# Optimization experiments

Hardware: AMD Instinct MI355X
Metric: run time of the kernel (lower is better)

The kernel has to match this reference:

```python
import jax, jax.numpy as jnp
import numpy as np

B, T, F = 256, 512, 8
H = 512
OUT = 96


def setup_inputs() -> dict:
    key = jax.random.key(0)
    ks = jax.random.split(key, 7)
    stdv = 1.0 / np.sqrt(H)
    u = lambda k, shape, s: jax.random.uniform(k, shape, jnp.float32, -s, s)
    return {
        "x": jax.random.normal(ks[0], (B, T, F), jnp.float32),
        "weight_ih": u(ks[1], (3 * H, F), stdv),
        "weight_hh": u(ks[2], (3 * H, H), stdv),
        "bias_ih": u(ks[3], (3 * H,), stdv),
        "bias_hh": u(ks[4], (3 * H,), stdv),
        "fc_w": u(ks[5], (OUT, H), 1.0 / np.sqrt(H)),
        "fc_b": u(ks[6], (OUT,), 1.0 / np.sqrt(H)),
    }


def _gru_last_hidden(x, weight_ih, weight_hh, bias_ih, bias_hh):
    # x: [B, T, F] (batch_first). Precompute input projections for all steps.
    xt = jnp.swapaxes(x, 0, 1)                      # [T, B, F]
    x_res = jnp.einsum('tbf,gf->tbg', xt, weight_ih) + bias_ih  # [T, B, 3H]
    h0 = jnp.zeros((x.shape[0], weight_hh.shape[1]), x.dtype)   # [B, H]

    def step(h, xr):
        h_res = h @ weight_hh.T + bias_hh           # [B, 3H]
        i_r, i_z, i_n = jnp.split(xr, 3, axis=1)
        h_r, h_z, h_n = jnp.split(h_res, 3, axis=1)
        r = jax.nn.sigmoid(i_r + h_r)
        z = jax.nn.sigmoid(i_z + h_z)
        n = jnp.tanh(i_n + r * h_n)
        h_new = n - n * z + z * h                   # = (1-z)*n + z*h
        return h_new, None

    h_last, _ = jax.lax.scan(step, h0, x_res)
    return h_last                                    # [B, H]


def reference(x, weight_ih, weight_hh, bias_ih, bias_hh, fc_w, fc_b):
    h_last = _gru_last_hidden(x, weight_ih, weight_hh, bias_ih, bias_hh)
    return h_last @ fc_w.T + fc_b                    # [B, OUT]
```

## Files before the change

kernel.cpp:

```cpp
#include <hip/hip_runtime.h>
#include <hip/hip_bf16.h>

#define B_ 256
#define T_ 512
#define F_ 8
#define H_ 512
#define OUT_ 96

#define NCL 16
#define BT 16
#define NWG 8

typedef __attribute__((ext_vector_type(8))) short short8;
typedef __attribute__((ext_vector_type(4))) float f32x4;

__device__ unsigned long long g_hbuf[2ull * 64 * 256 * 2];
__device__ __align__(64) unsigned g_flag[NCL * 16];

__device__ __forceinline__ short f2bf(float v) {
  __hip_bfloat16 b = __float2bfloat16(v);
  unsigned short u;
  __builtin_memcpy(&u, &b, 2);
  return (short)u;
}

__device__ __forceinline__ size_t hidx(int buf, int chunk, int row) {
  return ((size_t)((buf * 64 + chunk) * 256 + row)) * 2;
}

__global__ void init_flags() {
  int i = blockIdx.x * 256 + (int)threadIdx.x;
  if (i < NCL * 16) g_flag[i] = 0;
}

__global__ __launch_bounds__(256, 1) void gru_persistent(
    const float* x, const float* w_ih, const float* w_hh,
    const float* bias_ih, const float* bias_hh,
    const float* fc_w, const float* fc_b, float* out) {
  const int tid = (int)threadIdx.x;
  const int w = tid >> 6;
  const int lane = tid & 63;
  const int l15 = lane & 15;
  const int lg = lane >> 4;
  const int bid = (int)blockIdx.x;
  const int cl = bid & 15;
  const int wgj = bid >> 4;
  const int rb0 = cl * BT;
  const int c0 = wgj * 64 + w * 16;

  __shared__ short8 h_lds[1024];
  __shared__ short t_h[16][68];

  short8 wfrag[3][17];
#pragma unroll
  for (int g = 0; g < 3; ++g) {
    const float* wr = w_hh + (size_t)(g * H_ + c0 + l15) * H_ + lg * 8;
#pragma unroll
    for (int kk = 0; kk < 16; ++kk) {
      f32x4 a = ((const f32x4*)(wr + kk * 32))[0];
      f32x4 b2 = ((const f32x4*)(wr + kk * 32))[1];
      short8 o;
#pragma unroll
      for (int j = 0; j < 4; ++j) { o[j] = f2bf(a[j]); o[4 + j] = f2bf(b2[j]); }
      wfrag[g][kk] = o;
    }
    short8 o = {0, 0, 0, 0, 0, 0, 0, 0};
    if (lg == 0) {
      const f32x4* wi = (const f32x4*)(w_ih + (size_t)(g * H_ + c0 + l15) * F_);
      f32x4 a = wi[0], b2 = wi[1];
#pragma unroll
      for (int j = 0; j < 4; ++j) { o[j] = f2bf(a[j]); o[4 + j] = f2bf(b2[j]); }
    }
    wfrag[g][16] = o;
  }

  const int colh = c0 + l15;
  const float b_r = bias_ih[colh] + bias_hh[colh];
  const float b_z = bias_ih[H_ + colh] + bias_hh[H_ + colh];
  const float bin_ = bias_ih[2 * H_ + colh];
  const float bhn_ = bias_hh[2 * H_ + colh];

  float hown[4] = {0.f, 0.f, 0.f, 0.f};
  bool gaveup = false;

  const int hrow = rb0 + l15;
  const float* xrow = x + (size_t)hrow * T_ * F_;

  f32x4 xa = ((const f32x4*)xrow)[0];
  f32x4 xb2 = ((const f32x4*)xrow)[1];

  for (int t = 0; t < T_; ++t) {
    if (t > 0) {
      if (!gaveup) {
        unsigned spins = 0;
        for (;;) {
          unsigned f = __hip_atomic_load(&g_flag[cl * 16 + (lane & 7)],
                                         __ATOMIC_RELAXED, __HIP_MEMORY_SCOPE_AGENT);
          if (__all((int)(f >= (unsigned)t))) break;
          __builtin_amdgcn_s_sleep(2);
          if (++spins > (1u << 20)) { gaveup = true; break; }
        }
        __builtin_amdgcn_sched_barrier(0);
      }
      const int buf = t & 1;
#pragma unroll
      for (int r4 = 0; r4 < 4; ++r4) {
        const int idx = r4 * 256 + tid;
        const int chunk = idx >> 4;
        const int lr = idx & 15;
        size_t i0 = hidx(buf, chunk, rb0 + lr);
        unsigned long long q0 = __hip_atomic_load(&g_hbuf[i0], __ATOMIC_RELAXED,
                                                  __HIP_MEMORY_SCOPE_AGENT);
        unsigned long long q1 = __hip_atomic_load(&g_hbuf[i0 + 1], __ATOMIC_RELAXED,
                                                  __HIP_MEMORY_SCOPE_AGENT);
        union { unsigned long long q[2]; short8 s; } u;
        u.q[0] = q0; u.q[1] = q1;
        h_lds[idx] = u.s;
      }
    }

    short8 xf;
#pragma unroll
    for (int j = 0; j < 4; ++j) { xf[j] = f2bf(xa[j]); xf[4 + j] = f2bf(xb2[j]); }

    __syncthreads();

    {
      const int tn = (t + 1 < T_) ? t + 1 : T_ - 1;
      xa = ((const f32x4*)(xrow + (size_t)tn * F_))[0];
      xb2 = ((const f32x4*)(xrow + (size_t)tn * F_))[1];
    }

    f32x4 acc_r = {0.f, 0.f, 0.f, 0.f}, acc_z = {0.f, 0.f, 0.f, 0.f};
    f32x4 acc_nh = {0.f, 0.f, 0.f, 0.f}, acc_nx = {0.f, 0.f, 0.f, 0.f};
    if (t > 0) {
#pragma unroll
      for (int kk = 0; kk < 16; ++kk) {
        short8 a = h_lds[(kk * 4 + lg) * 16 + l15];
        acc_r = __builtin_amdgcn_mfma_f32_16x16x32_bf16(a, wfrag[0][kk], acc_r, 0, 0, 0);
        acc_z = __builtin_amdgcn_mfma_f32_16x16x32_bf16(a, wfrag[1][kk], acc_z, 0, 0, 0);
        acc_nh = __builtin_amdgcn_mfma_f32_16x16x32_bf16(a, wfrag[2][kk], acc_nh, 0, 0, 0);
      }
    }
    acc_r = __builtin_amdgcn_mfma_f32_16x16x32_bf16(xf, wfrag[0][16], acc_r, 0, 0, 0);
    acc_z = __builtin_amdgcn_mfma_f32_16x16x32_bf16(xf, wfrag[1][16], acc_z, 0, 0, 0);
    acc_nx = __builtin_amdgcn_mfma_f32_16x16x32_bf16(xf, wfrag[2][16], acc_nx, 0, 0, 0);

    short hnew[4];
#pragma unroll
    for (int q = 0; q < 4; ++q) {
      float pr = acc_r[q] + b_r;
      float pz = acc_z[q] + b_z;
      float r = 1.f / (1.f + __expf(-pr));
      float z = 1.f / (1.f + __expf(-pz));
      float n = tanhf(acc_nx[q] + bin_ + r * (acc_nh[q] + bhn_));
      hown[q] = n + z * (hown[q] - n);
      hnew[q] = f2bf(hown[q]);
    }

#pragma unroll
    for (int q = 0; q < 4; ++q) t_h[4 * lg + q][w * 16 + l15] = hnew[q];
    __syncthreads();
    {
      const int row_l = tid >> 4;
      const int ucol = tid & 15;
      const int col = wgj * 64 + ucol * 4;
      const int grow = rb0 + row_l;
      unsigned long long v;
      __builtin_memcpy(&v, &t_h[row_l][ucol * 4], 8);
      size_t i0 = hidx((t + 1) & 1, col >> 3, grow) + ((col >> 2) & 1);
      __hip_atomic_store(&g_hbuf[i0], v, __ATOMIC_RELAXED, __HIP_MEMORY_SCOPE_AGENT);
    }
    __syncthreads();
    if (tid == 0)
      __hip_atomic_store(&g_flag[cl * 16 + wgj], (unsigned)(t + 1),
                         __ATOMIC_RELAXED, __HIP_MEMORY_SCOPE_AGENT);
  }

  const int wi = wgj * 4 + w;
  if (wi >= OUT_ / 16) return;
  if (!gaveup) {
    unsigned spins = 0;
    for (;;) {
      unsigned f = __hip_atomic_load(&g_flag[cl * 16 + (lane & 7)],
                                     __ATOMIC_RELAXED, __HIP_MEMORY_SCOPE_AGENT);
      if (__all((int)(f >= (unsigned)T_))) break;
      __builtin_amdgcn_s_sleep(2);
      if (++spins > (1u << 20)) break;
    }
    __builtin_amdgcn_fence(__ATOMIC_ACQUIRE, "agent");
  }
  short8 afrag[16];
#pragma unroll
  for (int kk = 0; kk < 16; ++kk) {
    size_t i0 = hidx(0, kk * 4 + lg, hrow);
    unsigned long long q0 =
        __hip_atomic_load(&g_hbuf[i0], __ATOMIC_RELAXED, __HIP_MEMORY_SCOPE_AGENT);
    unsigned long long q1 =
        __hip_atomic_load(&g_hbuf[i0 + 1], __ATOMIC_RELAXED, __HIP_MEMORY_SCOPE_AGENT);
    union { unsigned long long q[2]; short8 s; } u;
    u.q[0] = q0; u.q[1] = q1;
    afrag[kk] = u.s;
  }
  const int col = wi * 16 + l15;
  const float* wrow = fc_w + (size_t)col * H_ + lg * 8;
  f32x4 acc = {0.f, 0.f, 0.f, 0.f};
#pragma unroll
  for (int kk = 0; kk < 16; ++kk) {
    f32x4 a = ((const f32x4*)(wrow + kk * 32))[0];
    f32x4 b2 = ((const f32x4*)(wrow + kk * 32))[1];
    short8 bfr;
#pragma unroll
    for (int j = 0; j < 4; ++j) { bfr[j] = f2bf(a[j]); bfr[4 + j] = f2bf(b2[j]); }
    acc = __builtin_amdgcn_mfma_f32_16x16x32_bf16(afrag[kk], bfr, acc, 0, 0, 0);
  }
  const float fb = fc_b[col];
#pragma unroll
  for (int q = 0; q < 4; ++q) {
    int row_o = rb0 + lg * 4 + q;
    out[(size_t)row_o * OUT_ + col] = acc[q] + fb;
  }
}

extern "C" void kernel_launch(void* const* d_in, const int* in_sizes, int n_in,
                              void* d_out, int out_size, void* d_ws, size_t ws_size,
                              hipStream_t stream) {
  const float* x = (const float*)d_in[0];
  const float* w_ih = (const float*)d_in[1];
  const float* w_hh = (const float*)d_in[2];
  const float* b_ih = (const float*)d_in[3];
  const float* b_hh = (const float*)d_in[4];
  const float* fc_w = (const float*)d_in[5];
  const float* fc_b = (const float*)d_in[6];

  init_flags<<<1, 256, 0, stream>>>();
  gru_persistent<<<NCL * NWG, 256, 0, stream>>>(x, w_ih, w_hh, b_ih, b_hh,
                                                fc_w, fc_b, (float*)d_out);
}
```

Measured before the change: 1.723 ms.

## Publish hidden state per wavefront with per-wave flags, dropping block barriers

Each wavefront now stages its own 16x16 hidden tile in a private LDS slice, stores it to global memory, waits for the stores to complete, and raises its own flag. This replaces the two workgroup-wide barriers and the single per-workgroup flag. Consumers poll 32 per-wave flags instead of 8, and the sleep in the step spin-loop is removed. The aim is to cut barrier and signalling latency on the serial recurrence critical path, at the cost of more flag traffic and busier polling.

```diff
diff --git a/kernel.cpp b/kernel.cpp
--- a/kernel.cpp
+++ b/kernel.cpp
@@ -15,7 +15,7 @@
 typedef __attribute__((ext_vector_type(4))) float f32x4;
 
 __device__ unsigned long long g_hbuf[2ull * 64 * 256 * 2];
-__device__ __align__(64) unsigned g_flag[NCL * 16];
+__device__ __align__(128) unsigned g_flag[NCL * 32];
 
 __device__ __forceinline__ short f2bf(float v) {
   __hip_bfloat16 b = __float2bfloat16(v);
@@ -30,7 +30,7 @@
 
 __global__ void init_flags() {
   int i = blockIdx.x * 256 + (int)threadIdx.x;
-  if (i < NCL * 16) g_flag[i] = 0;
+  if (i < NCL * 32) g_flag[i] = 0;
 }
 
 __global__ __launch_bounds__(256, 1) void gru_persistent(
@@ -49,7 +49,7 @@
   const int c0 = wgj * 64 + w * 16;
 
   __shared__ short8 h_lds[1024];
-  __shared__ short t_h[16][68];
+  __shared__ short t_hw[4][16][18];
 
   short8 wfrag[3][17];
 #pragma unroll
@@ -82,6 +82,8 @@
 
   float hown[4] = {0.f, 0.f, 0.f, 0.f};
   bool gaveup = false;
+  unsigned* flags = &g_flag[cl * 32];
+  const int wflag = wgj * 4 + w;
 
   const int hrow = rb0 + l15;
   const float* xrow = x + (size_t)hrow * T_ * F_;
@@ -94,10 +96,9 @@
       if (!gaveup) {
         unsigned spins = 0;
         for (;;) {
-          unsigned f = __hip_atomic_load(&g_flag[cl * 16 + (lane & 7)],
-                                         __ATOMIC_RELAXED, __HIP_MEMORY_SCOPE_AGENT);
+          unsigned f = __hip_atomic_load(&flags[lane & 31], __ATOMIC_RELAXED,
+                                         __HIP_MEMORY_SCOPE_AGENT);
           if (__all((int)(f >= (unsigned)t))) break;
-          __builtin_amdgcn_s_sleep(2);
           if (++spins > (1u << 20)) { gaveup = true; break; }
         }
         __builtin_amdgcn_sched_barrier(0);
@@ -106,9 +107,7 @@
 #pragma unroll
       for (int r4 = 0; r4 < 4; ++r4) {
         const int idx = r4 * 256 + tid;
-        const int chunk = idx >> 4;
-        const int lr = idx & 15;
-        size_t i0 = hidx(buf, chunk, rb0 + lr);
+        size_t i0 = hidx(buf, idx >> 4, rb0 + (idx & 15));
         unsigned long long q0 = __hip_atomic_load(&g_hbuf[i0], __ATOMIC_RELAXED,
                                                   __HIP_MEMORY_SCOPE_AGENT);
         unsigned long long q1 = __hip_atomic_load(&g_hbuf[i0 + 1], __ATOMIC_RELAXED,
@@ -159,22 +158,20 @@
     }
 
 #pragma unroll
-    for (int q = 0; q < 4; ++q) t_h[4 * lg + q][w * 16 + l15] = hnew[q];
-    __syncthreads();
+    for (int q = 0; q < 4; ++q) t_hw[w][4 * lg + q][l15] = hnew[q];
     {
-      const int row_l = tid >> 4;
-      const int ucol = tid & 15;
-      const int col = wgj * 64 + ucol * 4;
-      const int grow = rb0 + row_l;
+      const int r = lane >> 2;
+      const int cq = lane & 3;
       unsigned long long v;
-      __builtin_memcpy(&v, &t_h[row_l][ucol * 4], 8);
-      size_t i0 = hidx((t + 1) & 1, col >> 3, grow) + ((col >> 2) & 1);
+      __builtin_memcpy(&v, &t_hw[w][r][cq * 4], 8);
+      const int colg = c0 + cq * 4;
+      size_t i0 = hidx((t + 1) & 1, colg >> 3, rb0 + r) + ((colg >> 2) & 1);
       __hip_atomic_store(&g_hbuf[i0], v, __ATOMIC_RELAXED, __HIP_MEMORY_SCOPE_AGENT);
     }
-    __syncthreads();
-    if (tid == 0)
-      __hip_atomic_store(&g_flag[cl * 16 + wgj], (unsigned)(t + 1),
-                         __ATOMIC_RELAXED, __HIP_MEMORY_SCOPE_AGENT);
+    asm volatile("s_waitcnt vmcnt(0)" ::: "memory");
+    if (lane == 0)
+      __hip_atomic_store(&flags[wflag], (unsigned)(t + 1), __ATOMIC_RELAXED,
+                         __HIP_MEMORY_SCOPE_AGENT);
   }
 
   const int wi = wgj * 4 + w;
@@ -182,10 +179,10 @@
   if (!gaveup) {
     unsigned spins = 0;
     for (;;) {
-      unsigned f = __hip_atomic_load(&g_flag[cl * 16 + (lane & 7)],
-                                     __ATOMIC_RELAXED, __HIP_MEMORY_SCOPE_AGENT);
+      unsigned f = __hip_atomic_load(&flags[lane & 31], __ATOMIC_RELAXED,
+                                     __HIP_MEMORY_SCOPE_AGENT);
       if (__all((int)(f >= (unsigned)T_))) break;
-      __builtin_amdgcn_s_sleep(2);
+      __builtin_amdgcn_s_sleep(1);
       if (++spins > (1u << 20)) break;
     }
     __builtin_amdgcn_fence(__ATOMIC_ACQUIRE, "agent");
```

After: 2.068 ms. 1.2x slower.

## Replace flag-based step sync with timestep-tagged hidden-state words

Applied to the files above, without the earlier changes.

Each bf16 hidden value is now stored in a 32-bit slot whose upper 16 bits carry the timestep, so consumers poll the data itself instead of a separate per-cluster flag array. This removes the two workgroup barriers and the flag store per step, and merges flag polling with the data fetch into one round trip. Hidden writes now go out per wave directly from a small per-wave LDS tile. The cost is doubled global traffic for hidden state, plus 16-bit tags that would wrap if T exceeded 65535. Readiness also rests on each 64-bit tagged store being seen atomically, with no acquire fence.

```diff
diff --git a/kernel.cpp b/kernel.cpp
--- a/kernel.cpp
+++ b/kernel.cpp
@@ -14,8 +14,7 @@
 typedef __attribute__((ext_vector_type(8))) short short8;
 typedef __attribute__((ext_vector_type(4))) float f32x4;
 
-__device__ unsigned long long g_hbuf[2ull * 64 * 256 * 2];
-__device__ __align__(64) unsigned g_flag[NCL * 16];
+__device__ unsigned long long g_ht[2][NCL][16][256];
 
 __device__ __forceinline__ short f2bf(float v) {
   __hip_bfloat16 b = __float2bfloat16(v);
@@ -24,13 +23,10 @@
   return (short)u;
 }
 
-__device__ __forceinline__ size_t hidx(int buf, int chunk, int row) {
-  return ((size_t)((buf * 64 + chunk) * 256 + row)) * 2;
-}
-
-__global__ void init_flags() {
+__global__ void init_ht() {
   int i = blockIdx.x * 256 + (int)threadIdx.x;
-  if (i < NCL * 16) g_flag[i] = 0;
+  unsigned long long* p = &g_ht[0][0][0][0];
+  __hip_atomic_store(&p[i], 0ull, __ATOMIC_RELAXED, __HIP_MEMORY_SCOPE_AGENT);
 }
 
 __global__ __launch_bounds__(256, 1) void gru_persistent(
@@ -49,7 +45,7 @@
   const int c0 = wgj * 64 + w * 16;
 
   __shared__ short8 h_lds[1024];
-  __shared__ short t_h[16][68];
+  __shared__ short t_hw[4][16][20];
 
   short8 wfrag[3][17];
 #pragma unroll
@@ -83,39 +79,51 @@
   float hown[4] = {0.f, 0.f, 0.f, 0.f};
   bool gaveup = false;
 
-  const int hrow = rb0 + l15;
-  const float* xrow = x + (size_t)hrow * T_ * F_;
+  const float* xrow = x + (size_t)(rb0 + l15) * T_ * F_;
+
+  const int grow = tid & 15;
+  const int gcp = (tid >> 4) * 4;
+  const int prow = lane >> 2;
+  const int pcp = (c0 >> 1) + (lane & 3) * 2;
 
   f32x4 xa = ((const f32x4*)xrow)[0];
   f32x4 xb2 = ((const f32x4*)xrow)[1];
 
   for (int t = 0; t < T_; ++t) {
     if (t > 0) {
+      const unsigned long long tagw = (unsigned long long)t;
+      const int buf = t & 1;
+      unsigned long long vv[16];
       if (!gaveup) {
         unsigned spins = 0;
         for (;;) {
-          unsigned f = __hip_atomic_load(&g_flag[cl * 16 + (lane & 7)],
-                                         __ATOMIC_RELAXED, __HIP_MEMORY_SCOPE_AGENT);
-          if (__all((int)(f >= (unsigned)t))) break;
-          __builtin_amdgcn_s_sleep(2);
+          unsigned long long bad = 0;
+#pragma unroll
+          for (int i = 0; i < 16; ++i) {
+            const int r4 = i >> 2, k = i & 3;
+            vv[i] = __hip_atomic_load(&g_ht[buf][cl][grow][gcp + r4 * 64 + k],
+                                      __ATOMIC_RELAXED, __HIP_MEMORY_SCOPE_AGENT);
+            bad |= (((vv[i] >> 16) ^ tagw) & 0xFFFFull) | ((vv[i] >> 48) ^ tagw);
+          }
+          if (!bad) break;
           if (++spins > (1u << 20)) { gaveup = true; break; }
+          __builtin_amdgcn_s_sleep(1);
         }
-        __builtin_amdgcn_sched_barrier(0);
-      }
-      const int buf = t & 1;
+      } else {
+#pragma unroll
+        for (int i = 0; i < 16; ++i) {
+          const int r4 = i >> 2, k = i & 3;
+          vv[i] = __hip_atomic_load(&g_ht[buf][cl][grow][gcp + r4 * 64 + k],
+                                    __ATOMIC_RELAXED, __HIP_MEMORY_SCOPE_AGENT);
+        }
+      }
 #pragma unroll
       for (int r4 = 0; r4 < 4; ++r4) {
-        const int idx = r4 * 256 + tid;
-        const int chunk = idx >> 4;
-        const int lr = idx & 15;
-        size_t i0 = hidx(buf, chunk, rb0 + lr);
-        unsigned long long q0 = __hip_atomic_load(&g_hbuf[i0], __ATOMIC_RELAXED,
-                                                  __HIP_MEMORY_SCOPE_AGENT);
-        unsigned long long q1 = __hip_atomic_load(&g_hbuf[i0 + 1], __ATOMIC_RELAXED,
-                                                  __HIP_MEMORY_SCOPE_AGENT);
-        union { unsigned long long q[2]; short8 s; } u;
-        u.q[0] = q0; u.q[1] = q1;
-        h_lds[idx] = u.s;
+        short8 o;
+#pragma unroll
+        for (int j = 0; j < 8; ++j)
+          o[j] = (short)(vv[r4 * 4 + (j >> 1)] >> (32 * (j & 1)));
+        h_lds[r4 * 256 + tid] = o;
       }
     }
 
@@ -159,49 +167,56 @@
     }
 
 #pragma unroll
-    for (int q = 0; q < 4; ++q) t_h[4 * lg + q][w * 16 + l15] = hnew[q];
-    __syncthreads();
+    for (int q = 0; q < 4; ++q) t_hw[w][4 * lg + q][l15] = hnew[q];
     {
-      const int row_l = tid >> 4;
-      const int ucol = tid & 15;
-      const int col = wgj * 64 + ucol * 4;
-      const int grow = rb0 + row_l;
       unsigned long long v;
-      __builtin_memcpy(&v, &t_h[row_l][ucol * 4], 8);
-      size_t i0 = hidx((t + 1) & 1, col >> 3, grow) + ((col >> 2) & 1);
-      __hip_atomic_store(&g_hbuf[i0], v, __ATOMIC_RELAXED, __HIP_MEMORY_SCOPE_AGENT);
-    }
-    __syncthreads();
-    if (tid == 0)
-      __hip_atomic_store(&g_flag[cl * 16 + wgj], (unsigned)(t + 1),
-                         __ATOMIC_RELAXED, __HIP_MEMORY_SCOPE_AGENT);
-  }
-
+      __builtin_memcpy(&v, &t_hw[w][prow][(lane & 3) * 4], 8);
+      const unsigned long long tg = (unsigned long long)(t + 1) << 16;
+      unsigned long long w0 = (tg | (v & 0xFFFFull)) |
+                              ((tg | ((v >> 16) & 0xFFFFull)) << 32);
+      unsigned long long w1 = (tg | ((v >> 32) & 0xFFFFull)) |
+                              ((tg | ((v >> 48) & 0xFFFFull)) << 32);
+      const int pbuf = (t + 1) & 1;
+      __hip_atomic_store(&g_ht[pbuf][cl][prow][pcp], w0, __ATOMIC_RELAXED,
+                         __HIP_MEMORY_SCOPE_AGENT);
+      __hip_atomic_store(&g_ht[pbuf][cl][prow][pcp + 1], w1, __ATOMIC_RELAXED,
+                         __HIP_MEMORY_SCOPE_AGENT);
+    }
+  }
+
+  if (wgj >= 2) return;
+  {
+    const unsigned long long tagw = (unsigned long long)T_;
+    unsigned long long vv[16];
+    unsigned spins = 0;
+    for (;;) {
+      unsigned long long bad = 0;
+#pragma unroll
+      for (int i = 0; i < 16; ++i) {
+        const int r4 = i >> 2, k = i & 3;
+        vv[i] = __hip_atomic_load(&g_ht[0][cl][grow][gcp + r4 * 64 + k],
+                                  __ATOMIC_RELAXED, __HIP_MEMORY_SCOPE_AGENT);
+        bad |= (((vv[i] >> 16) ^ tagw) & 0xFFFFull) | ((vv[i] >> 48) ^ tagw);
+      }
+      if (!bad) break;
+      if (++spins > (1u << 20)) break;
+      __builtin_amdgcn_s_sleep(1);
+    }
+#pragma unroll
+    for (int r4 = 0; r4 < 4; ++r4) {
+      short8 o;
+#pragma unroll
+      for (int j = 0; j < 8; ++j)
+        o[j] = (short)(vv[r4 * 4 + (j >> 1)] >> (32 * (j & 1)));
+      h_lds[r4 * 256 + tid] = o;
+    }
+  }
+  __syncthreads();
   const int wi = wgj * 4 + w;
   if (wi >= OUT_ / 16) return;
-  if (!gaveup) {
-    unsigned spins = 0;
-    for (;;) {
-      unsigned f = __hip_atomic_load(&g_flag[cl * 16 + (lane & 7)],
-                                     __ATOMIC_RELAXED, __HIP_MEMORY_SCOPE_AGENT);
-      if (__all((int)(f >= (unsigned)T_))) break;
-      __builtin_amdgcn_s_sleep(2);
-      if (++spins > (1u << 20)) break;
-    }
-    __builtin_amdgcn_fence(__ATOMIC_ACQUIRE, "agent");
-  }
   short8 afrag[16];
 #pragma unroll
-  for (int kk = 0; kk < 16; ++kk) {
-    size_t i0 = hidx(0, kk * 4 + lg, hrow);
-    unsigned long long q0 =
-        __hip_atomic_load(&g_hbuf[i0], __ATOMIC_RELAXED, __HIP_MEMORY_SCOPE_AGENT);
-    unsigned long long q1 =
-        __hip_atomic_load(&g_hbuf[i0 + 1], __ATOMIC_RELAXED, __HIP_MEMORY_SCOPE_AGENT);
-    union { unsigned long long q[2]; short8 s; } u;
-    u.q[0] = q0; u.q[1] = q1;
-    afrag[kk] = u.s;
-  }
+  for (int kk = 0; kk < 16; ++kk) afrag[kk] = h_lds[(kk * 4 + lg) * 16 + l15];
   const int col = wi * 16 + l15;
   const float* wrow = fc_w + (size_t)col * H_ + lg * 8;
   f32x4 acc = {0.f, 0.f, 0.f, 0.f};
@@ -233,7 +248,7 @@
   const float* fc_w = (const float*)d_in[5];
   const float* fc_b = (const float*)d_in[6];
 
-  init_flags<<<1, 256, 0, stream>>>();
+  init_ht<<<512, 256, 0, stream>>>();
   gru_persistent<<<NCL * NWG, 256, 0, stream>>>(x, w_ih, w_hh, b_ih, b_hh,
                                                 fc_w, fc_b, (float*)d_out);
 }
```

Measured after the change: 3.274 ms. +90.0%, slower.
